# Optimization experiments

Hardware: AMD Instinct MI355X
Metric: run time of the kernel (lower is better)

Reference implementation:

```python
import jax, jax.numpy as jnp
import numpy as np

NEG_SLOPE = 0.2
EPS = 1e-16


def _add_self_loops(edge_index, edge_weight, N):
    # PyG add_self_loops with fill_value='mean': self-loop attr = mean of
    # incoming edge attrs per node (0 if node has no incoming edges).
    src, dst = edge_index[0], edge_index[1]
    ones = jnp.ones_like(edge_weight)
    cnt = jax.ops.segment_sum(ones, dst, num_segments=N)
    wsum = jax.ops.segment_sum(edge_weight, dst, num_segments=N)
    self_w = jnp.where(cnt > 0, wsum / jnp.maximum(cnt, 1.0), 0.0)
    loop = jnp.arange(N, dtype=src.dtype)
    return (jnp.concatenate([src, loop]), jnp.concatenate([dst, loop]),
            jnp.concatenate([edge_weight, self_w]))


def _gatv2_layer(x, src, dst, ew, Wl, Wr, att, We, bias, N):
    # x: [M, N, Din]; src/dst: [E']; ew: [E']; att: [H, C]
    M = x.shape[0]
    H, C = att.shape
    xl = (x @ Wl).reshape(M, N, H, C)   # source transform (lin_l)
    xr = (x @ Wr).reshape(M, N, H, C)   # target transform (lin_r)
    xj = xl[:, src]                      # [M, E', H, C] gather source feats
    xi = xr[:, dst]                      # [M, E', H, C] gather target feats
    ee = (ew[:, None] @ We).reshape(-1, H, C)  # [E', H, C] edge embedding
    s = jax.nn.leaky_relu(xi + xj + ee[None], NEG_SLOPE)
    logits = jnp.einsum('mehc,hc->meh', s, att)  # [M, E', H]
    # segment softmax over edges grouped by destination node
    smax = jax.vmap(lambda u: jax.ops.segment_max(u, dst, num_segments=N))(logits)
    a = jnp.exp(logits - smax[:, dst])
    denom = jax.vmap(lambda u: jax.ops.segment_sum(u, dst, num_segments=N))(a)
    alpha = a / (denom[:, dst] + EPS)
    msg = alpha[..., None] * xj          # [M, E', H, C]
    out = jax.vmap(lambda u: jax.ops.segment_sum(u, dst, num_segments=N))(msg)
    return out.reshape(M, N, H * C) + bias


def setup_inputs() -> dict:
    key = jax.random.key(0)
    ks = jax.random.split(key, 14)
    B, T, N, Din = 2, 8, 5000, 64
    E, H, OUT = 80000, 2, 128
    C = OUT // H  # 64
    g = jax.nn.initializers.glorot_uniform()
    inp = {
        'x': jax.random.normal(ks[0], (B, T, N, Din), jnp.float32),
        'edge_index': jax.random.randint(ks[1], (2, E), 0, N, jnp.int32),
        'edge_weight': jax.random.uniform(ks[2], (E,), jnp.float32),
        # conv1 params
        'Wl1': g(ks[3], (Din, H * C), jnp.float32),
        'Wr1': g(ks[4], (Din, H * C), jnp.float32),
        'att1': g(ks[5], (H, C), jnp.float32),
        'We1': g(ks[6], (1, H * C), jnp.float32),
        'b1': jnp.zeros((H * C,), jnp.float32),
        # conv2 params
        'Wl2': g(ks[7], (OUT, H * C), jnp.float32),
        'Wr2': g(ks[8], (OUT, H * C), jnp.float32),
        'att2': g(ks[9], (H, C), jnp.float32),
        'We2': g(ks[10], (1, H * C), jnp.float32),
        'b2': jnp.zeros((H * C,), jnp.float32),
    }
    return inp


def reference(x, edge_index, edge_weight, Wl1, Wr1, att1, We1, b1,
              Wl2, Wr2, att2, We2, b2):
    B, T, N, Din = x.shape
    M = B * T
    # Tiling edges by B*T with node offsets is equivalent to sharing the same
    # edge list across M independent graph copies -> vectorize over M.
    src, dst, ew = _add_self_loops(edge_index, edge_weight, N)
    h = x.reshape(M, N, Din)
    h = _gatv2_layer(h, src, dst, ew, Wl1, Wr1, att1, We1, b1, N)
    h = jax.nn.elu(h)
    h = _gatv2_layer(h, src, dst, ew, Wl2, Wr2, att2, We2, b2, N)
    h = jax.nn.elu(h)
    return h.reshape(B, T, N, -1)
```

## Files before the change

kernel.cpp:

```cpp
#include <hip/hip_runtime.h>
#include <cstdint>
#include <cstddef>

static constexpr float NEG_SLOPE_C = 0.2f;
static constexpr float EPS_C = 1e-16f;
static constexpr float LOG2E_C = 1.4426950408889634f;

#if defined(__has_builtin)
#if __has_builtin(__builtin_amdgcn_exp2f)
#define EXP2F(x) __builtin_amdgcn_exp2f(x)
#else
#define EXP2F(x) exp2f(x)
#endif
#else
#define EXP2F(x) exp2f(x)
#endif

typedef __attribute__((ext_vector_type(8))) short bf16x8;
typedef __attribute__((ext_vector_type(4))) float f32x4;
typedef __attribute__((ext_vector_type(2))) float f32x2;

__device__ __forceinline__ f32x2 pk_add(f32x2 a, f32x2 b) {
    f32x2 d;
    asm("v_pk_add_f32 %0, %1, %2" : "=v"(d) : "v"(a), "v"(b));
    return d;
}
__device__ __forceinline__ f32x2 pk_mul(f32x2 a, f32x2 b) {
    f32x2 d;
    asm("v_pk_mul_f32 %0, %1, %2" : "=v"(d) : "v"(a), "v"(b));
    return d;
}
__device__ __forceinline__ f32x2 pk_fma(f32x2 a, f32x2 b, f32x2 c) {
    f32x2 d;
    asm("v_pk_fma_f32 %0, %1, %2, %3" : "=v"(d) : "v"(a), "v"(b), "v"(c));
    return d;
}
__device__ __forceinline__ f32x2 pk_abs(f32x2 a) {
    f32x2 d;
    d.x = __builtin_fabsf(a.x);
    d.y = __builtin_fabsf(a.y);
    return d;
}

__device__ __forceinline__ short bf16_rne(float x) {
    unsigned u = __float_as_uint(x);
    u = (u + 0x7FFF + ((u >> 16) & 1)) >> 16;
    return (short)u;
}
__device__ __forceinline__ float bf16f(short s) {
    return __uint_as_float(((unsigned)(unsigned short)s) << 16);
}

template<int CTRL>
__device__ __forceinline__ float dpp_add_f(float v) {
    int x = __builtin_amdgcn_update_dpp(0, __float_as_int(v), CTRL, 0xf, 0xf, true);
    return v + __int_as_float(x);
}

__device__ __forceinline__ float reduce16(float q) {
    q = dpp_add_f<0xB1>(q);
    q = dpp_add_f<0x4E>(q);
    q = dpp_add_f<0x141>(q);
    q = dpp_add_f<0x140>(q);
    return q;
}


__global__ void degree_kernel(const int* __restrict__ ei, const float* __restrict__ ew,
                              int E, int* __restrict__ cnt, float* __restrict__ wsum) {
    int e = blockIdx.x * blockDim.x + threadIdx.x;
    if (e >= E) return;
    int dst = ei[E + e];
    atomicAdd(&cnt[dst], 1);
    atomicAdd(&wsum[dst], ew[e]);
}

__global__ void scan_kernel(const int* __restrict__ cnt, const float* __restrict__ wsum,
                            int N, int E, int* __restrict__ offs, float* __restrict__ self_w) {
    __shared__ int bufA[1024];
    __shared__ int bufB[1024];
    int t = threadIdx.x;
    int chunk = (N + 1023) / 1024;
    int lo = t * chunk;
    int hi = lo + chunk; if (hi > N) hi = N; if (lo > N) lo = N;
    int s = 0;
    for (int n = lo; n < hi; ++n) s += cnt[n];
    bufA[t] = s;
    __syncthreads();
    int* srcb = bufA; int* dstb = bufB;
    for (int d = 1; d < 1024; d <<= 1) {
        int v = srcb[t];
        if (t >= d) v += srcb[t - d];
        dstb[t] = v;
        __syncthreads();
        int* tmp = srcb; srcb = dstb; dstb = tmp;
    }
    int run = (t == 0) ? 0 : srcb[t - 1];
    for (int n = lo; n < hi; ++n) { offs[n] = run; run += cnt[n]; }
    if (t == 0) offs[N] = E;
    for (int n = t; n < N; n += 1024) {
        int c = cnt[n];
        self_w[n] = (c > 0) ? (wsum[n] / (float)c) : 0.0f;
    }
}

__global__ void scatter_kernel(const int* __restrict__ ei, const float* __restrict__ ew, int E,
                               const int* __restrict__ offs, int* __restrict__ cursor,
                               int4* __restrict__ pairs) {
    int e = blockIdx.x * blockDim.x + threadIdx.x;
    if (e >= E) return;
    int dst = ei[E + e];
    int pos = offs[dst] + atomicAdd(&cursor[dst], 1);
    int wb = __float_as_int(ew[e]);
    pairs[pos] = make_int4(ei[e] * 512, 0, wb, wb);
}


template<int K>
__global__ void wprep_kernel(const float* __restrict__ Wl, const float* __restrict__ Wr,
                             uint4* __restrict__ Wf) {
    const int gid = blockIdx.x * 256 + threadIdx.x;
    const int lane = gid & 63;
    const int t = (gid >> 6) & 15;
    const int s = gid >> 10;
    const int mr = lane & 15, q = lane >> 4;
    const int col = t * 16 + mr;
    const float* src = (col < 128) ? (Wl + col) : (Wr + col - 128);
    union { short sh[8]; uint4 u; } hv, lv;
    #pragma unroll
    for (int j = 0; j < 8; ++j) {
        const float v = src[(size_t)(s * 32 + q * 8 + j) * 128];
        const short h = bf16_rne(v);
        hv.sh[j] = h;
        lv.sh[j] = bf16_rne(v - bf16f(h));
    }
    const size_t base = (size_t)s * 2048 + (size_t)(t * 2) * 64 + lane;
    Wf[base] = hv.u;
    Wf[base + 64] = lv.u;
}


template<int K>
__global__ __launch_bounds__(256) void gemm_mfma_kernel(
    const float* __restrict__ X, const uint4* __restrict__ Wf,
    float* __restrict__ outL, float* __restrict__ outR) {
    __shared__ uint4 wbuf[2048];
    const int tid = threadIdx.x;
    const int wv = tid >> 6;
    const int lane = tid & 63;
    const int q = lane >> 4;
    const int mr = lane & 15;
    const int xrow = blockIdx.x * 64 + wv * 16 + mr;

    f32x4 acc[16];
    #pragma unroll
    for (int t = 0; t < 16; ++t) acc[t] = (f32x4){0.f, 0.f, 0.f, 0.f};

    const float* xp = X + (size_t)xrow * K + q * 8;

    for (int s = 0; s < K / 32; ++s) {
        const float4 a0 = *(const float4*)(xp + s * 32);
        const float4 a1 = *(const float4*)(xp + s * 32 + 4);

        __syncthreads();
        const uint4* gsrc = Wf + (size_t)s * 2048 + wv * 512 + lane;
        #pragma unroll
        for (int i = 0; i < 8; ++i)
            wbuf[wv * 512 + i * 64 + lane] = gsrc[i * 64];
        __syncthreads();

        const float av[8] = {a0.x, a0.y, a0.z, a0.w, a1.x, a1.y, a1.z, a1.w};
        bf16x8 xh, xl;
        #pragma unroll
        for (int j = 0; j < 8; ++j) {
            const short h = bf16_rne(av[j]);
            xh[j] = h;
            xl[j] = bf16_rne(av[j] - bf16f(h));
        }
        #pragma unroll
        for (int t = 0; t < 16; ++t) {
            const bf16x8 wh = *(const bf16x8*)&wbuf[(t * 2) * 64 + lane];
            const bf16x8 wl = *(const bf16x8*)&wbuf[(t * 2 + 1) * 64 + lane];
            acc[t] = __builtin_amdgcn_mfma_f32_16x16x32_bf16(wh, xh, acc[t], 0, 0, 0);
            acc[t] = __builtin_amdgcn_mfma_f32_16x16x32_bf16(wl, xh, acc[t], 0, 0, 0);
            acc[t] = __builtin_amdgcn_mfma_f32_16x16x32_bf16(wh, xl, acc[t], 0, 0, 0);
        }
    }

    const size_t ob = (size_t)xrow * 128 + q * 4;
    #pragma unroll
    for (int t = 0; t < 8; ++t) {
        *(float4*)(outL + ob + t * 16) =
            make_float4(acc[t][0], acc[t][1], acc[t][2], acc[t][3]);
        *(float4*)(outR + ob + t * 16) =
            make_float4(acc[t + 8][0], acc[t + 8][1], acc[t + 8][2], acc[t + 8][3]);
    }
}


__global__ __launch_bounds__(256) void edge_kernel(
    const float* __restrict__ xl, const float* __restrict__ xr,
    const int* __restrict__ offs, const int4* __restrict__ pairs,
    const float* __restrict__ self_w,
    const float* __restrict__ att, const float* __restrict__ We,
    const float* __restrict__ bias, float* __restrict__ out,
    int N, int M) {
    const int wave = __builtin_amdgcn_readfirstlane(threadIdx.x >> 6);
    const int b = blockIdx.x;
    const int hb = (b >= 10000) ? (b - 10000) : b;
    const int m = ((b >= 10000) ? 8 : 0) + (hb & 7);
    const int n = (hb >> 3) * 4 + wave;
    if (n >= N) return;
    const int lane = threadIdx.x & 63;
    const int j = lane & 31;
    const bool hi = lane >= 32;
    const int h4 = (lane >> 5) << 2;
    const int j16 = j << 4;

    const char* xlp = (const char*)(xl + (size_t)m * N * 128);
    const char* xrp = (const char*)(xr + (size_t)m * N * 128);

    const int beg = offs[n], end = offs[n + 1];
    const int last = end - 1;
    const bool any = end > beg;

    int4 myp;
    if (any) myp = pairs[min(beg + lane, last)];

    f32x2 a06_01, a06_23, a04_01, a04_23, we01, we23, xi01, xi23;
    {
        const float4 at4 = ((const float4*)att)[j];
        const float4 we4 = ((const float4*)We)[j];
        const float4 xi4 = *(const float4*)(xrp + (size_t)n * 512 + j16);
        const float c06 = 0.6f * LOG2E_C, c04 = 0.4f * LOG2E_C;
        a06_01 = (f32x2){at4.x * c06, at4.y * c06};
        a06_23 = (f32x2){at4.z * c06, at4.w * c06};
        a04_01 = (f32x2){at4.x * c04, at4.y * c04};
        a04_23 = (f32x2){at4.z * c04, at4.w * c04};
        we01 = (f32x2){we4.x, we4.y};
        we23 = (f32x2){we4.z, we4.w};
        xi01 = (f32x2){xi4.x, xi4.y};
        xi23 = (f32x2){xi4.z, xi4.w};
    }

    float base, lsum;
    f32x2 acc01, acc23;
    {
        const float sw = self_w[n];
        const f32x2 sw2 = (f32x2){sw, sw};
        const float4 xj4 = *(const float4*)(xlp + (size_t)n * 512 + j16);
        const f32x2 s01 = pk_fma(sw2, we01, pk_add(xi01, (f32x2){xj4.x, xj4.y}));
        const f32x2 s23 = pk_fma(sw2, we23, pk_add(xi23, (f32x2){xj4.z, xj4.w}));
        f32x2 q01 = pk_mul(a06_01, s01);
        q01 = pk_fma(a04_01, pk_abs(s01), q01);
        f32x2 q23 = pk_mul(a06_23, s23);
        q23 = pk_fma(a04_23, pk_abs(s23), q23);
        const f32x2 qp = pk_add(q01, q23);
        base = reduce16(qp.x + qp.y);
        lsum = 0.5f;
        acc01 = (f32x2){xj4.x * 0.5f, xj4.y * 0.5f};
        acc23 = (f32x2){xj4.z * 0.5f, xj4.w * 0.5f};
    }

    auto BODY = [&](f32x2 w2, float4 xj4, bool mask) {
        const f32x2 xj01 = (f32x2){xj4.x, xj4.y};
        const f32x2 xj23 = (f32x2){xj4.z, xj4.w};
        const f32x2 s01 = pk_fma(w2, we01, pk_add(xi01, xj01));
        const f32x2 s23 = pk_fma(w2, we23, pk_add(xi23, xj23));
        f32x2 q01 = pk_mul(a06_01, s01);
        q01 = pk_fma(a04_01, pk_abs(s01), q01);
        f32x2 q23 = pk_mul(a06_23, s23);
        q23 = pk_fma(a04_23, pk_abs(s23), q23);
        const f32x2 qp = pk_add(q01, q23);
        const float q = reduce16(qp.x + qp.y);
        float t = EXP2F(q - base);
        if (mask) t = hi ? 0.f : t;
        lsum += t;
        const f32x2 t2 = (f32x2){t, t};
        acc01 = pk_fma(t2, xj01, acc01);
        acc23 = pk_fma(t2, xj23, acc23);
    };

    if (any) {
        for (int cbeg = beg; cbeg < end; cbeg += 64) {
            const int cdeg = min(end - cbeg, 64);
            const int niter = (cdeg + 1) >> 1;
            const bool odd = (cdeg & 1) != 0;

            auto PULL = [&](int s, int& ro, f32x2& w2) {
                const int idx = (s << 3) + h4;
                ro = __builtin_amdgcn_ds_bpermute(idx, myp.x);
                int wl = __builtin_amdgcn_ds_bpermute(idx, myp.z);
                int wh = __builtin_amdgcn_ds_bpermute(idx, myp.w);
                w2 = (f32x2){__int_as_float(wl), __int_as_float(wh)};
            };
            auto GATH = [&](int ro) -> float4 {
                return *(const float4*)(xlp + (unsigned)(ro + j16));
            };

            int roA, roB; f32x2 wA, wB;
            PULL(0, roA, wA);
            PULL(1, roB, wB);
            float4 xA = GATH(roA);
            float4 xB = GATH(roB);

            int k = 0;
            while (k + 2 < niter) {
                BODY(wA, xA, false);
                PULL(k + 2, roA, wA);
                xA = GATH(roA);
                BODY(wB, xB, false);
                PULL(k + 3, roB, wB);
                xB = GATH(roB);
                k += 2;
            }
            if (niter - k == 2) {
                BODY(wA, xA, false);
                BODY(wB, xB, odd);
            } else {
                BODY(wA, xA, odd);
            }

            if (cbeg + 64 < end)
                myp = pairs[min(cbeg + 64 + lane, last)];
        }
    }

    lsum += __shfl_xor(lsum, 32, 64);
    acc01.x += __shfl_xor(acc01.x, 32, 64);
    acc01.y += __shfl_xor(acc01.y, 32, 64);
    acc23.x += __shfl_xor(acc23.x, 32, 64);
    acc23.y += __shfl_xor(acc23.y, 32, 64);

    const float inv = 1.f / (lsum + EPS_C);
    const float4 b4 = ((const float4*)bias)[j];
    float o0 = fmaf(acc01.x, inv, b4.x);
    float o1 = fmaf(acc01.y, inv, b4.y);
    float o2 = fmaf(acc23.x, inv, b4.z);
    float o3 = fmaf(acc23.y, inv, b4.w);
    o0 = o0 > 0.f ? o0 : (__expf(o0) - 1.f);
    o1 = o1 > 0.f ? o1 : (__expf(o1) - 1.f);
    o2 = o2 > 0.f ? o2 : (__expf(o2) - 1.f);
    o3 = o3 > 0.f ? o3 : (__expf(o3) - 1.f);
    if (!hi) {
        ((float4*)(out + (size_t)m * N * 128))[n * 32 + j] =
            make_float4(o0, o1, o2, o3);
    }
}


extern "C" void kernel_launch(void* const* d_in, const int* in_sizes, int n_in,
                              void* d_out, int out_size, void* d_ws, size_t ws_size,
                              hipStream_t stream) {
    const float* x    = (const float*)d_in[0];
    const int*   ei   = (const int*)d_in[1];
    const float* ew   = (const float*)d_in[2];
    const float* Wl1  = (const float*)d_in[3];
    const float* Wr1  = (const float*)d_in[4];
    const float* att1 = (const float*)d_in[5];
    const float* We1  = (const float*)d_in[6];
    const float* b1   = (const float*)d_in[7];
    const float* Wl2  = (const float*)d_in[8];
    const float* Wr2  = (const float*)d_in[9];
    const float* att2 = (const float*)d_in[10];
    const float* We2  = (const float*)d_in[11];
    const float* b2   = (const float*)d_in[12];

    const int E = in_sizes[1] / 2;
    const int N = 5000;
    const int R = out_size / 128;
    const int M = R / N;

    char* ws = (char*)d_ws;
    size_t off = 0;
    auto alloc = [&](size_t bytes) {
        char* p = ws + off;
        off = (off + bytes + 255) & ~(size_t)255;
        return p;
    };
    int*   cnt    = (int*)  alloc((size_t)N * 4);
    float* wsum   = (float*)alloc((size_t)N * 4);
    float* selfw  = (float*)alloc((size_t)N * 4);
    int*   offs   = (int*)  alloc((size_t)(N + 1) * 4);
    int*   cursor = (int*)  alloc((size_t)N * 4);
    int4*  pairs  = (int4*) alloc((size_t)(E + 1) * 16);
    uint4* wf1    = (uint4*)alloc((size_t)2 * 2048 * 16);
    uint4* wf2    = (uint4*)alloc((size_t)4 * 2048 * 16);
    float* bufA   = (float*)alloc((size_t)R * 128 * 4);
    float* bufB   = (float*)alloc((size_t)R * 128 * 4);
    float* bufC   = (float*)alloc((size_t)R * 128 * 4);

    hipMemsetAsync(cnt,    0, (size_t)N * 4, stream);
    hipMemsetAsync(wsum,   0, (size_t)N * 4, stream);
    hipMemsetAsync(cursor, 0, (size_t)N * 4, stream);

    int eb = (E + 255) / 256;
    degree_kernel<<<eb, 256, 0, stream>>>(ei, ew, E, cnt, wsum);
    scan_kernel<<<1, 1024, 0, stream>>>(cnt, wsum, N, E, offs, selfw);
    scatter_kernel<<<eb, 256, 0, stream>>>(ei, ew, E, offs, cursor, pairs);
    wprep_kernel<64><<<8, 256, 0, stream>>>(Wl1, Wr1, wf1);
    wprep_kernel<128><<<16, 256, 0, stream>>>(Wl2, Wr2, wf2);

    const int gb = R / 64;
    const int tb = 2 * ((N + 3) / 4) * 8;

    gemm_mfma_kernel<64><<<gb, 256, 0, stream>>>(x, wf1, bufA, bufB);
    edge_kernel<<<tb, 256, 0, stream>>>(bufA, bufB, offs, pairs, selfw,
                                        att1, We1, b1, bufC, N, M);
    gemm_mfma_kernel<128><<<gb, 256, 0, stream>>>(bufC, wf2, bufA, bufB);
    edge_kernel<<<tb, 256, 0, stream>>>(bufA, bufB, offs, pairs, selfw,
                                        att2, We2, b2, (float*)d_out, N, M);
}
```

Baseline: 300.4 us.

## Compact edge pairs, deepen gather pipeline to four stages, merge memsets

Shrinks the per-edge CSR record from int4 to int2 (source offset and weight) and cuts one ds_bpermute per pulled edge. It deepens the edge-kernel gather software pipeline from two to four in-flight source-row loads, with sched_barriers to keep loads ahead of compute. It also merges three memsets into one by making the zeroed buffers contiguous. The trade-off is more registers per thread, which could reduce occupancy, and a more complex remainder-handling path.

```diff
diff --git a/kernel.cpp b/kernel.cpp
--- a/kernel.cpp
+++ b/kernel.cpp
@@ -106,13 +106,12 @@
 
 __global__ void scatter_kernel(const int* __restrict__ ei, const float* __restrict__ ew, int E,
                                const int* __restrict__ offs, int* __restrict__ cursor,
-                               int4* __restrict__ pairs) {
+                               int2* __restrict__ pairs) {
     int e = blockIdx.x * blockDim.x + threadIdx.x;
     if (e >= E) return;
     int dst = ei[E + e];
     int pos = offs[dst] + atomicAdd(&cursor[dst], 1);
-    int wb = __float_as_int(ew[e]);
-    pairs[pos] = make_int4(ei[e] * 512, 0, wb, wb);
+    pairs[pos] = make_int2(ei[e] * 512, __float_as_int(ew[e]));
 }
 
 
@@ -200,7 +199,7 @@
 
 __global__ __launch_bounds__(256) void edge_kernel(
     const float* __restrict__ xl, const float* __restrict__ xr,
-    const int* __restrict__ offs, const int4* __restrict__ pairs,
+    const int* __restrict__ offs, const int2* __restrict__ pairs,
     const float* __restrict__ self_w,
     const float* __restrict__ att, const float* __restrict__ We,
     const float* __restrict__ bias, float* __restrict__ out,
@@ -224,7 +223,7 @@
     const int last = end - 1;
     const bool any = end > beg;
 
-    int4 myp;
+    int2 myp;
     if (any) myp = pairs[min(beg + lane, last)];
 
     f32x2 a06_01, a06_23, a04_01, a04_23, we01, we23, xi01, xi23;
@@ -290,36 +289,49 @@
             auto PULL = [&](int s, int& ro, f32x2& w2) {
                 const int idx = (s << 3) + h4;
                 ro = __builtin_amdgcn_ds_bpermute(idx, myp.x);
-                int wl = __builtin_amdgcn_ds_bpermute(idx, myp.z);
-                int wh = __builtin_amdgcn_ds_bpermute(idx, myp.w);
-                w2 = (f32x2){__int_as_float(wl), __int_as_float(wh)};
+                const int wb = __builtin_amdgcn_ds_bpermute(idx, myp.y);
+                w2.x = __int_as_float(wb);
+                w2.y = w2.x;
             };
             auto GATH = [&](int ro) -> float4 {
                 return *(const float4*)(xlp + (unsigned)(ro + j16));
             };
 
-            int roA, roB; f32x2 wA, wB;
+            int roA, roB, roC, roD;
+            f32x2 wA, wB, wC, wD;
             PULL(0, roA, wA);
             PULL(1, roB, wB);
+            PULL(2, roC, wC);
+            PULL(3, roD, wD);
             float4 xA = GATH(roA);
             float4 xB = GATH(roB);
+            float4 xC, xD;
 
             int k = 0;
-            while (k + 2 < niter) {
+            while (k + 4 < niter) {
+                xC = GATH(roC);
+                xD = GATH(roD);
+                __builtin_amdgcn_sched_barrier(0);
                 BODY(wA, xA, false);
-                PULL(k + 2, roA, wA);
+                PULL(k + 4, roA, wA);
+                BODY(wB, xB, false);
+                PULL(k + 5, roB, wB);
                 xA = GATH(roA);
-                BODY(wB, xB, false);
-                PULL(k + 3, roB, wB);
                 xB = GATH(roB);
-                k += 2;
+                __builtin_amdgcn_sched_barrier(0);
+                BODY(wC, xC, false);
+                PULL(k + 6, roC, wC);
+                BODY(wD, xD, false);
+                PULL(k + 7, roD, wD);
+                k += 4;
             }
-            if (niter - k == 2) {
-                BODY(wA, xA, false);
-                BODY(wB, xB, odd);
-            } else {
-                BODY(wA, xA, odd);
-            }
+            const int rem = niter - k;
+            if (rem >= 3) xC = GATH(roC);
+            if (rem == 4) xD = GATH(roD);
+            BODY(wA, xA, odd && (rem == 1));
+            if (rem >= 2) BODY(wB, xB, odd && (rem == 2));
+            if (rem >= 3) BODY(wC, xC, odd && (rem == 3));
+            if (rem == 4) BODY(wD, xD, odd);
 
             if (cbeg + 64 < end)
                 myp = pairs[min(cbeg + 64 + lane, last)];
@@ -380,19 +392,18 @@
     };
     int*   cnt    = (int*)  alloc((size_t)N * 4);
     float* wsum   = (float*)alloc((size_t)N * 4);
+    int*   cursor = (int*)  alloc((size_t)N * 4);
     float* selfw  = (float*)alloc((size_t)N * 4);
     int*   offs   = (int*)  alloc((size_t)(N + 1) * 4);
-    int*   cursor = (int*)  alloc((size_t)N * 4);
-    int4*  pairs  = (int4*) alloc((size_t)(E + 1) * 16);
+    int2*  pairs  = (int2*) alloc((size_t)(E + 1) * 8);
     uint4* wf1    = (uint4*)alloc((size_t)2 * 2048 * 16);
     uint4* wf2    = (uint4*)alloc((size_t)4 * 2048 * 16);
     float* bufA   = (float*)alloc((size_t)R * 128 * 4);
     float* bufB   = (float*)alloc((size_t)R * 128 * 4);
     float* bufC   = (float*)alloc((size_t)R * 128 * 4);
 
-    hipMemsetAsync(cnt,    0, (size_t)N * 4, stream);
-    hipMemsetAsync(wsum,   0, (size_t)N * 4, stream);
-    hipMemsetAsync(cursor, 0, (size_t)N * 4, stream);
+    const size_t zspan = (size_t)((char*)cursor - (char*)cnt) + (size_t)N * 4;
+    hipMemsetAsync(cnt, 0, zspan, stream);
 
     int eb = (E + 255) / 256;
     degree_kernel<<<eb, 256, 0, stream>>>(ei, ew, E, cnt, wsum);
```

Result: faster. 291.9 us (-2.8%).
